# Performance work log

Hardware: AMD Instinct MI355X
Metric: run time of the kernel (lower is better)

## Reference

```python
import jax, jax.numpy as jnp
import numpy as np

B, T, N, D = 16, 48, 256, 64
K_HEADS = 8


def setup_inputs() -> dict:
    key = jax.random.key(0)
    ks = jax.random.split(key, 12)
    return {
        "query": jax.random.normal(ks[0], (B, T, N, D), jnp.float32),
        "key": jax.random.normal(ks[1], (B, T, N, D), jnp.float32),
        "value": jax.random.normal(ks[2], (B, T, N, D), jnp.float32),
        "key_w": jax.random.normal(ks[3], (B, T, D, D), jnp.float32) * 0.05,
        "key_b": jax.random.normal(ks[4], (B, T, D), jnp.float32) * 0.05,
        "value_w": jax.random.normal(ks[5], (B, T, D, D), jnp.float32) * 0.05,
        "value_b": jax.random.normal(ks[6], (B, T, D), jnp.float32) * 0.05,
        "proj1_w": jax.random.normal(ks[7], (D, D), jnp.float32) * 0.05,
        "proj1_b": jax.random.normal(ks[8], (D,), jnp.float32) * 0.05,
        "proj2_w": jax.random.normal(ks[9], (D, D), jnp.float32) * 0.05,
        "proj2_b": jax.random.normal(ks[10], (D,), jnp.float32) * 0.05,
        "rate": jnp.full((1,), 0.8, jnp.float32),
    }


def reference(query, key, value, key_w, key_b, value_w, value_b,
              proj1_w, proj1_b, proj2_w, proj2_b, rate):
    b, t, n, d = query.shape
    hs = d // K_HEADS
    # per-(batch,time) projections (LinearCustom)
    k = jnp.einsum('btnd,btde->btne', key, key_w) + key_b[:, :, None, :]
    v = jnp.einsum('btnd,btde->btne', value, value_w) + value_b[:, :, None, :]
    # split heads along channel dim (matches torch.split on dim -1)
    qh = query.reshape(b, t, n, K_HEADS, hs)
    kh = k.reshape(b, t, n, K_HEADS, hs)
    vh = v.reshape(b, t, n, K_HEADS, hs)
    # scores: [b, h, n, q, k]
    scores = jnp.einsum('bqnhd,bknhd->bhnqk', qh, kh) / jnp.sqrt(jnp.asarray(hs, query.dtype))
    # time decay: b_time_decays[..., i, j] = (T-1-i) + 1 = T - i (depends on query pos only)
    dec = (t - jnp.arange(t, dtype=scores.dtype))[:, None]  # [T, 1], broadcasts over key axis
    s = jax.nn.sigmoid(scores)
    denom = 1.0 + jax.nn.sigmoid(s * jax.nn.sigmoid(rate) * dec)
    att = jax.nn.softmax(jnp.tanh(s / denom), axis=-1)
    x = jnp.einsum('bhnqk,bknhd->bqnhd', att, vh).reshape(b, t, n, d)
    x = jnp.tanh(x @ proj1_w.T + proj1_b)
    return x @ proj2_w.T + proj2_b
```

## Files before the change

### kernel.cpp

```cpp
#include <hip/hip_runtime.h>


#define B_ 16
#define T_ 48
#define N_ 256
#define D_ 64
#define H_ 8
#define HS_ 8

__device__ __forceinline__ float rcpf(float x) { return __builtin_amdgcn_rcpf(x); }
__device__ __forceinline__ float ex2(float x) { return __builtin_amdgcn_exp2f(x); }

#define LOG2E 1.4426950408889634f

__global__ __launch_bounds__(256) void proj_kv_kernel(
    const float* __restrict__ key, const float* __restrict__ key_w, const float* __restrict__ key_b,
    const float* __restrict__ value, const float* __restrict__ value_w, const float* __restrict__ value_b,
    float* __restrict__ k_out, float* __restrict__ v_out)
{
    const int bt = blockIdx.x;
    const int which = blockIdx.y;
    const float* __restrict__ in = (which ? value : key) + (size_t)bt * N_ * D_;
    const float* __restrict__ w  = (which ? value_w : key_w) + (size_t)bt * D_ * D_;
    const float* __restrict__ bb = (which ? value_b : key_b) + (size_t)bt * D_;
    float* __restrict__ out = (which ? v_out : k_out) + (size_t)bt * N_ * D_;

    __shared__ float Wl[D_][D_];
    __shared__ float Xl[128][68];
    __shared__ float Bl[D_];

    const int tid = threadIdx.x;
    #pragma unroll
    for (int i = tid; i < D_ * D_; i += 256) Wl[i >> 6][i & 63] = w[i];
    if (tid < D_) Bl[tid] = bb[tid];

    const int cg = tid & 7;
    const int rg = tid >> 3;

    for (int n0 = 0; n0 < N_; n0 += 128) {
        __syncthreads();
        #pragma unroll
        for (int i = tid; i < 128 * D_ / 4; i += 256) {
            const int e = i * 4;
            *(float4*)&Xl[e >> 6][e & 63] = *(const float4*)&in[(size_t)n0 * D_ + e];
        }
        __syncthreads();

        float acc[4][8];
        #pragma unroll
        for (int j = 0; j < 4; ++j)
            #pragma unroll
            for (int i = 0; i < 8; ++i) acc[j][i] = Bl[cg * 8 + i];

        #pragma unroll 8
        for (int d = 0; d < D_; ++d) {
            const float4 w0 = *(const float4*)&Wl[d][cg * 8];
            const float4 w1 = *(const float4*)&Wl[d][cg * 8 + 4];
            #pragma unroll
            for (int j = 0; j < 4; ++j) {
                const float a = Xl[rg + 32 * j][d];
                acc[j][0] += a * w0.x; acc[j][1] += a * w0.y;
                acc[j][2] += a * w0.z; acc[j][3] += a * w0.w;
                acc[j][4] += a * w1.x; acc[j][5] += a * w1.y;
                acc[j][6] += a * w1.z; acc[j][7] += a * w1.w;
            }
        }

        #pragma unroll
        for (int j = 0; j < 4; ++j) {
            const size_t row = (size_t)(n0 + rg + 32 * j);
            *(float4*)&out[row * D_ + cg * 8]     = make_float4(acc[j][0], acc[j][1], acc[j][2], acc[j][3]);
            *(float4*)&out[row * D_ + cg * 8 + 4] = make_float4(acc[j][4], acc[j][5], acc[j][6], acc[j][7]);
        }
    }
}

__global__ __launch_bounds__(384) void attn_kernel(
    const float* __restrict__ query, float* __restrict__ k_xatt, const float* __restrict__ v_in,
    const float* __restrict__ rate)
{
    const int b = blockIdx.x >> 8;
    const int n = blockIdx.x & 255;

    __shared__ float Q[T_][68];
    __shared__ float K[T_][68];
    __shared__ float V[T_][68];

    const int tid = threadIdx.x;
    #pragma unroll
    for (int i = tid; i < T_ * D_ / 4; i += 384) {
        const int e = i * 4;
        const int t = e >> 6, d = e & 63;
        const size_t g = ((size_t)(b * T_ + t) * N_ + n) * D_ + d;
        *(float4*)&Q[t][d] = *(const float4*)&query[g];
        *(float4*)&K[t][d] = *(const float4*)&k_xatt[g];
        *(float4*)&V[t][d] = *(const float4*)&v_in[g];
    }
    const float rsig = rcpf(1.0f + ex2(-rate[0] * LOG2E));
    __syncthreads();

    const int q = tid % 48;
    const int h = tid / 48;

    const float C1 = 0.35355339059327373f * LOG2E;
    float4 qa = *(const float4*)&Q[q][h * 8];
    float4 qb = *(const float4*)&Q[q][h * 8 + 4];
    qa.x *= -C1; qa.y *= -C1; qa.z *= -C1; qa.w *= -C1;
    qb.x *= -C1; qb.y *= -C1; qb.z *= -C1; qb.w *= -C1;
    const float rdn = -rsig * (float)(T_ - q) * LOG2E;

    float4 acc0 = make_float4(0.f, 0.f, 0.f, 0.f);
    float4 acc1 = make_float4(0.f, 0.f, 0.f, 0.f);
    float ssum = 0.f;
    #pragma unroll 4
    for (int tk = 0; tk < T_; ++tk) {
        const float4 ka = *(const float4*)&K[tk][h * 8];
        const float4 kb = *(const float4*)&K[tk][h * 8 + 4];
        const float dn = qa.x * ka.x + qa.y * ka.y + qa.z * ka.z + qa.w * ka.w
                       + qb.x * kb.x + qb.y * kb.y + qb.z * kb.z + qb.w * kb.w;
        const float s   = rcpf(1.0f + ex2(dn));
        const float s2  = rcpf(1.0f + ex2(s * rdn));
        const float arg = s * rcpf(1.0f + s2);
        const float th  = 1.0f - 2.0f * rcpf(ex2(arg * (2.0f * LOG2E)) + 1.0f);
        const float e   = ex2(th * LOG2E);
        ssum += e;
        const float4 va = *(const float4*)&V[tk][h * 8];
        const float4 vb = *(const float4*)&V[tk][h * 8 + 4];
        acc0.x += e * va.x; acc0.y += e * va.y; acc0.z += e * va.z; acc0.w += e * va.w;
        acc1.x += e * vb.x; acc1.y += e * vb.y; acc1.z += e * vb.z; acc1.w += e * vb.w;
    }
    const float inv = rcpf(ssum);

    __syncthreads();
    acc0.x *= inv; acc0.y *= inv; acc0.z *= inv; acc0.w *= inv;
    acc1.x *= inv; acc1.y *= inv; acc1.z *= inv; acc1.w *= inv;
    *(float4*)&Q[q][h * 8]     = acc0;
    *(float4*)&Q[q][h * 8 + 4] = acc1;
    __syncthreads();

    #pragma unroll
    for (int i = tid; i < T_ * D_ / 4; i += 384) {
        const int e = i * 4;
        const int t = e >> 6, d = e & 63;
        *(float4*)&k_xatt[((size_t)(b * T_ + t) * N_ + n) * D_ + d] = *(const float4*)&Q[t][d];
    }
}

__global__ __launch_bounds__(512) void out_proj_kernel(
    const float* __restrict__ xatt,
    const float* __restrict__ p1w, const float* __restrict__ p1b,
    const float* __restrict__ p2w, const float* __restrict__ p2b,
    float* __restrict__ out)
{
    __shared__ float W1t[D_][68];
    __shared__ float W2t[D_][68];
    __shared__ float X[128][68];
    __shared__ float B1[D_], B2[D_];

    const int tid = threadIdx.x;
    const size_t m0 = (size_t)blockIdx.x * 128;

    #pragma unroll
    for (int i = tid; i < D_ * D_; i += 512) {
        const int c = i >> 6, d = i & 63;
        W1t[d][c] = p1w[i];
        W2t[d][c] = p2w[i];
    }
    #pragma unroll
    for (int i = tid; i < 128 * D_ / 4; i += 512) {
        const int e = i * 4;
        *(float4*)&X[e >> 6][e & 63] = *(const float4*)&xatt[m0 * D_ + e];
    }
    if (tid < D_) { B1[tid] = p1b[tid]; B2[tid] = p2b[tid]; }
    __syncthreads();

    const int cg = tid & 7;
    const int rp = tid >> 3;

    float x1a[8], x1b[8];
    {
        float a[8], b2r[8];
        #pragma unroll
        for (int i = 0; i < 8; ++i) { a[i] = B1[cg * 8 + i]; b2r[i] = B1[cg * 8 + i]; }
        #pragma unroll 8
        for (int d = 0; d < D_; ++d) {
            const float xv0 = X[rp][d];
            const float xv1 = X[rp + 64][d];
            const float4 w0 = *(const float4*)&W1t[d][cg * 8];
            const float4 w1 = *(const float4*)&W1t[d][cg * 8 + 4];
            a[0] += xv0 * w0.x; a[1] += xv0 * w0.y; a[2] += xv0 * w0.z; a[3] += xv0 * w0.w;
            a[4] += xv0 * w1.x; a[5] += xv0 * w1.y; a[6] += xv0 * w1.z; a[7] += xv0 * w1.w;
            b2r[0] += xv1 * w0.x; b2r[1] += xv1 * w0.y; b2r[2] += xv1 * w0.z; b2r[3] += xv1 * w0.w;
            b2r[4] += xv1 * w1.x; b2r[5] += xv1 * w1.y; b2r[6] += xv1 * w1.z; b2r[7] += xv1 * w1.w;
        }
        #pragma unroll
        for (int i = 0; i < 8; ++i) {
            x1a[i] = 1.0f - 2.0f * rcpf(ex2(a[i]   * (2.0f * LOG2E)) + 1.0f);
            x1b[i] = 1.0f - 2.0f * rcpf(ex2(b2r[i] * (2.0f * LOG2E)) + 1.0f);
        }
    }
    __syncthreads();
    #pragma unroll
    for (int i = 0; i < 8; ++i) {
        X[rp][cg * 8 + i]      = x1a[i];
        X[rp + 64][cg * 8 + i] = x1b[i];
    }
    __syncthreads();

    {
        float a[8], b2r[8];
        #pragma unroll
        for (int i = 0; i < 8; ++i) { a[i] = B2[cg * 8 + i]; b2r[i] = B2[cg * 8 + i]; }
        #pragma unroll 8
        for (int d = 0; d < D_; ++d) {
            const float xv0 = X[rp][d];
            const float xv1 = X[rp + 64][d];
            const float4 w0 = *(const float4*)&W2t[d][cg * 8];
            const float4 w1 = *(const float4*)&W2t[d][cg * 8 + 4];
            a[0] += xv0 * w0.x; a[1] += xv0 * w0.y; a[2] += xv0 * w0.z; a[3] += xv0 * w0.w;
            a[4] += xv0 * w1.x; a[5] += xv0 * w1.y; a[6] += xv0 * w1.z; a[7] += xv0 * w1.w;
            b2r[0] += xv1 * w0.x; b2r[1] += xv1 * w0.y; b2r[2] += xv1 * w0.z; b2r[3] += xv1 * w0.w;
            b2r[4] += xv1 * w1.x; b2r[5] += xv1 * w1.y; b2r[6] += xv1 * w1.z; b2r[7] += xv1 * w1.w;
        }
        const size_t og0 = (m0 + rp) * D_ + cg * 8;
        const size_t og1 = (m0 + rp + 64) * D_ + cg * 8;
        *(float4*)&out[og0]     = make_float4(a[0], a[1], a[2], a[3]);
        *(float4*)&out[og0 + 4] = make_float4(a[4], a[5], a[6], a[7]);
        *(float4*)&out[og1]     = make_float4(b2r[0], b2r[1], b2r[2], b2r[3]);
        *(float4*)&out[og1 + 4] = make_float4(b2r[4], b2r[5], b2r[6], b2r[7]);
    }
}

extern "C" void kernel_launch(void* const* d_in, const int* in_sizes, int n_in,
                              void* d_out, int out_size, void* d_ws, size_t ws_size,
                              hipStream_t stream) {
    const float* query   = (const float*)d_in[0];
    const float* key     = (const float*)d_in[1];
    const float* value   = (const float*)d_in[2];
    const float* key_w   = (const float*)d_in[3];
    const float* key_b   = (const float*)d_in[4];
    const float* value_w = (const float*)d_in[5];
    const float* value_b = (const float*)d_in[6];
    const float* p1w     = (const float*)d_in[7];
    const float* p1b     = (const float*)d_in[8];
    const float* p2w     = (const float*)d_in[9];
    const float* p2b     = (const float*)d_in[10];
    const float* rate    = (const float*)d_in[11];
    float* out = (float*)d_out;

    float* kws = (float*)d_ws;
    float* vws = kws + (size_t)B_ * T_ * N_ * D_;

    dim3 gridA(B_ * T_, 2);
    proj_kv_kernel<<<gridA, 256, 0, stream>>>(key, key_w, key_b, value, value_w, value_b, kws, vws);
    attn_kernel<<<B_ * N_, 384, 0, stream>>>(query, kws, vws, rate);
    out_proj_kernel<<<(B_ * T_ * N_) / 128, 512, 0, stream>>>(kws, p1w, p1b, p2w, p2b, out);
}
```

Measured before the change: 222.8 us.

## Register-tile attention over four queries per thread and enlarge out-proj tiles

The attention kernel now gives each block two nodes and each thread four queries of one head. Each K/V row read from shared memory is reused across four query computations, queries are read straight from global memory, and outputs are written directly. The output projection kernel drops to 128 threads, each computing an 8x8 register tile with float4 X loads, which raises reuse of each shared-memory read. The cost is higher register pressure and fewer threads per block, which may reduce occupancy and latency hiding, especially with the exp-heavy attention loop.

```diff
diff --git a/kernel.cpp b/kernel.cpp
--- a/kernel.cpp
+++ b/kernel.cpp
@@ -75,159 +75,197 @@
     }
 }
 
-__global__ __launch_bounds__(384) void attn_kernel(
+__global__ __launch_bounds__(192) void attn_kernel(
     const float* __restrict__ query, float* __restrict__ k_xatt, const float* __restrict__ v_in,
     const float* __restrict__ rate)
 {
-    const int b = blockIdx.x >> 8;
-    const int n = blockIdx.x & 255;
-
-    __shared__ float Q[T_][68];
-    __shared__ float K[T_][68];
-    __shared__ float V[T_][68];
+    const int b  = blockIdx.x >> 7;
+    const int n0 = (blockIdx.x & 127) * 2;
+
+    __shared__ float K[2][T_][D_];
+    __shared__ float V[2][T_][D_];
 
     const int tid = threadIdx.x;
     #pragma unroll
-    for (int i = tid; i < T_ * D_ / 4; i += 384) {
-        const int e = i * 4;
-        const int t = e >> 6, d = e & 63;
-        const size_t g = ((size_t)(b * T_ + t) * N_ + n) * D_ + d;
-        *(float4*)&Q[t][d] = *(const float4*)&query[g];
-        *(float4*)&K[t][d] = *(const float4*)&k_xatt[g];
-        *(float4*)&V[t][d] = *(const float4*)&v_in[g];
+    for (int i = tid; i < T_ * 16; i += 192) {
+        const int t = i >> 4, d4 = (i & 15) * 4;
+        const size_t g0 = ((size_t)(b * T_ + t) * N_ + n0) * D_ + d4;
+        *(float4*)&K[0][t][d4] = *(const float4*)&k_xatt[g0];
+        *(float4*)&V[0][t][d4] = *(const float4*)&v_in[g0];
+        *(float4*)&K[1][t][d4] = *(const float4*)&k_xatt[g0 + D_];
+        *(float4*)&V[1][t][d4] = *(const float4*)&v_in[g0 + D_];
     }
     const float rsig = rcpf(1.0f + ex2(-rate[0] * LOG2E));
-    __syncthreads();
-
-    const int q = tid % 48;
-    const int h = tid / 48;
+
+    const int nl  = tid / 96;
+    const int r96 = tid % 96;
+    const int qg  = r96 >> 3;
+    const int h   = r96 & 7;
+    const int n   = n0 + nl;
 
     const float C1 = 0.35355339059327373f * LOG2E;
-    float4 qa = *(const float4*)&Q[q][h * 8];
-    float4 qb = *(const float4*)&Q[q][h * 8 + 4];
-    qa.x *= -C1; qa.y *= -C1; qa.z *= -C1; qa.w *= -C1;
-    qb.x *= -C1; qb.y *= -C1; qb.z *= -C1; qb.w *= -C1;
-    const float rdn = -rsig * (float)(T_ - q) * LOG2E;
-
-    float4 acc0 = make_float4(0.f, 0.f, 0.f, 0.f);
-    float4 acc1 = make_float4(0.f, 0.f, 0.f, 0.f);
-    float ssum = 0.f;
-    #pragma unroll 4
+    float4 qa[4], qb[4];
+    float rdn[4];
+    #pragma unroll
+    for (int j = 0; j < 4; ++j) {
+        const int q = qg + 12 * j;
+        const size_t g = ((size_t)(b * T_ + q) * N_ + n) * D_ + h * 8;
+        const float4 a = *(const float4*)&query[g];
+        const float4 c = *(const float4*)&query[g + 4];
+        qa[j] = make_float4(-C1 * a.x, -C1 * a.y, -C1 * a.z, -C1 * a.w);
+        qb[j] = make_float4(-C1 * c.x, -C1 * c.y, -C1 * c.z, -C1 * c.w);
+        rdn[j] = -rsig * (float)(T_ - q) * LOG2E;
+    }
+    __syncthreads();
+
+    float4 acc0[4], acc1[4];
+    float ssum[4];
+    #pragma unroll
+    for (int j = 0; j < 4; ++j) {
+        acc0[j] = make_float4(0.f, 0.f, 0.f, 0.f);
+        acc1[j] = make_float4(0.f, 0.f, 0.f, 0.f);
+        ssum[j] = 0.f;
+    }
+
+    #pragma unroll 2
     for (int tk = 0; tk < T_; ++tk) {
-        const float4 ka = *(const float4*)&K[tk][h * 8];
-        const float4 kb = *(const float4*)&K[tk][h * 8 + 4];
-        const float dn = qa.x * ka.x + qa.y * ka.y + qa.z * ka.z + qa.w * ka.w
-                       + qb.x * kb.x + qb.y * kb.y + qb.z * kb.z + qb.w * kb.w;
-        const float s   = rcpf(1.0f + ex2(dn));
-        const float s2  = rcpf(1.0f + ex2(s * rdn));
-        const float arg = s * rcpf(1.0f + s2);
-        const float th  = 1.0f - 2.0f * rcpf(ex2(arg * (2.0f * LOG2E)) + 1.0f);
-        const float e   = ex2(th * LOG2E);
-        ssum += e;
-        const float4 va = *(const float4*)&V[tk][h * 8];
-        const float4 vb = *(const float4*)&V[tk][h * 8 + 4];
-        acc0.x += e * va.x; acc0.y += e * va.y; acc0.z += e * va.z; acc0.w += e * va.w;
-        acc1.x += e * vb.x; acc1.y += e * vb.y; acc1.z += e * vb.z; acc1.w += e * vb.w;
-    }
-    const float inv = rcpf(ssum);
-
-    __syncthreads();
-    acc0.x *= inv; acc0.y *= inv; acc0.z *= inv; acc0.w *= inv;
-    acc1.x *= inv; acc1.y *= inv; acc1.z *= inv; acc1.w *= inv;
-    *(float4*)&Q[q][h * 8]     = acc0;
-    *(float4*)&Q[q][h * 8 + 4] = acc1;
-    __syncthreads();
-
-    #pragma unroll
-    for (int i = tid; i < T_ * D_ / 4; i += 384) {
-        const int e = i * 4;
-        const int t = e >> 6, d = e & 63;
-        *(float4*)&k_xatt[((size_t)(b * T_ + t) * N_ + n) * D_ + d] = *(const float4*)&Q[t][d];
-    }
-}
-
-__global__ __launch_bounds__(512) void out_proj_kernel(
+        const float4 ka = *(const float4*)&K[nl][tk][h * 8];
+        const float4 kb = *(const float4*)&K[nl][tk][h * 8 + 4];
+        const float4 va = *(const float4*)&V[nl][tk][h * 8];
+        const float4 vb = *(const float4*)&V[nl][tk][h * 8 + 4];
+        #pragma unroll
+        for (int j = 0; j < 4; ++j) {
+            const float dn = qa[j].x * ka.x + qa[j].y * ka.y + qa[j].z * ka.z + qa[j].w * ka.w
+                           + qb[j].x * kb.x + qb[j].y * kb.y + qb[j].z * kb.z + qb[j].w * kb.w;
+            const float s   = rcpf(1.0f + ex2(dn));
+            const float s2  = rcpf(1.0f + ex2(s * rdn[j]));
+            const float arg = s * rcpf(1.0f + s2);
+            const float th  = 1.0f - 2.0f * rcpf(ex2(arg * (2.0f * LOG2E)) + 1.0f);
+            const float e   = ex2(th * LOG2E);
+            ssum[j] += e;
+            acc0[j].x += e * va.x; acc0[j].y += e * va.y; acc0[j].z += e * va.z; acc0[j].w += e * va.w;
+            acc1[j].x += e * vb.x; acc1[j].y += e * vb.y; acc1[j].z += e * vb.z; acc1[j].w += e * vb.w;
+        }
+    }
+
+    #pragma unroll
+    for (int j = 0; j < 4; ++j) {
+        const float inv = rcpf(ssum[j]);
+        const int q = qg + 12 * j;
+        const size_t g = ((size_t)(b * T_ + q) * N_ + n) * D_ + h * 8;
+        *(float4*)&k_xatt[g]     = make_float4(acc0[j].x * inv, acc0[j].y * inv, acc0[j].z * inv, acc0[j].w * inv);
+        *(float4*)&k_xatt[g + 4] = make_float4(acc1[j].x * inv, acc1[j].y * inv, acc1[j].z * inv, acc1[j].w * inv);
+    }
+}
+
+__global__ __launch_bounds__(128) void out_proj_kernel(
     const float* __restrict__ xatt,
     const float* __restrict__ p1w, const float* __restrict__ p1b,
     const float* __restrict__ p2w, const float* __restrict__ p2b,
     float* __restrict__ out)
 {
+    __shared__ float X[128][68];
     __shared__ float W1t[D_][68];
     __shared__ float W2t[D_][68];
-    __shared__ float X[128][68];
     __shared__ float B1[D_], B2[D_];
 
     const int tid = threadIdx.x;
     const size_t m0 = (size_t)blockIdx.x * 128;
 
     #pragma unroll
-    for (int i = tid; i < D_ * D_; i += 512) {
+    for (int i = tid; i < D_ * D_; i += 128) {
         const int c = i >> 6, d = i & 63;
         W1t[d][c] = p1w[i];
         W2t[d][c] = p2w[i];
     }
     #pragma unroll
-    for (int i = tid; i < 128 * D_ / 4; i += 512) {
-        const int e = i * 4;
-        *(float4*)&X[e >> 6][e & 63] = *(const float4*)&xatt[m0 * D_ + e];
+    for (int i = tid; i < 128 * 16; i += 128) {
+        const int row = i >> 4, d4 = (i & 15) * 4;
+        *(float4*)&X[row][d4] = *(const float4*)&xatt[(m0 + row) * D_ + d4];
     }
     if (tid < D_) { B1[tid] = p1b[tid]; B2[tid] = p2b[tid]; }
     __syncthreads();
 
     const int cg = tid & 7;
-    const int rp = tid >> 3;
-
-    float x1a[8], x1b[8];
+    const int rg = tid >> 3;
+
+    float x1[8][8];
     {
-        float a[8], b2r[8];
-        #pragma unroll
-        for (int i = 0; i < 8; ++i) { a[i] = B1[cg * 8 + i]; b2r[i] = B1[cg * 8 + i]; }
-        #pragma unroll 8
-        for (int d = 0; d < D_; ++d) {
-            const float xv0 = X[rp][d];
-            const float xv1 = X[rp + 64][d];
-            const float4 w0 = *(const float4*)&W1t[d][cg * 8];
-            const float4 w1 = *(const float4*)&W1t[d][cg * 8 + 4];
-            a[0] += xv0 * w0.x; a[1] += xv0 * w0.y; a[2] += xv0 * w0.z; a[3] += xv0 * w0.w;
-            a[4] += xv0 * w1.x; a[5] += xv0 * w1.y; a[6] += xv0 * w1.z; a[7] += xv0 * w1.w;
-            b2r[0] += xv1 * w0.x; b2r[1] += xv1 * w0.y; b2r[2] += xv1 * w0.z; b2r[3] += xv1 * w0.w;
-            b2r[4] += xv1 * w1.x; b2r[5] += xv1 * w1.y; b2r[6] += xv1 * w1.z; b2r[7] += xv1 * w1.w;
-        }
-        #pragma unroll
-        for (int i = 0; i < 8; ++i) {
-            x1a[i] = 1.0f - 2.0f * rcpf(ex2(a[i]   * (2.0f * LOG2E)) + 1.0f);
-            x1b[i] = 1.0f - 2.0f * rcpf(ex2(b2r[i] * (2.0f * LOG2E)) + 1.0f);
-        }
-    }
-    __syncthreads();
-    #pragma unroll
-    for (int i = 0; i < 8; ++i) {
-        X[rp][cg * 8 + i]      = x1a[i];
-        X[rp + 64][cg * 8 + i] = x1b[i];
+        float acc[8][8];
+        #pragma unroll
+        for (int j = 0; j < 8; ++j)
+            #pragma unroll
+            for (int i = 0; i < 8; ++i) acc[j][i] = B1[cg * 8 + i];
+
+        #pragma unroll 4
+        for (int d0 = 0; d0 < D_; d0 += 4) {
+            float4 w0[4], w1[4];
+            #pragma unroll
+            for (int dd = 0; dd < 4; ++dd) {
+                w0[dd] = *(const float4*)&W1t[d0 + dd][cg * 8];
+                w1[dd] = *(const float4*)&W1t[d0 + dd][cg * 8 + 4];
+            }
+            #pragma unroll
+            for (int j = 0; j < 8; ++j) {
+                const float4 xv = *(const float4*)&X[rg + 16 * j][d0];
+                acc[j][0] += xv.x * w0[0].x + xv.y * w0[1].x + xv.z * w0[2].x + xv.w * w0[3].x;
+                acc[j][1] += xv.x * w0[0].y + xv.y * w0[1].y + xv.z * w0[2].y + xv.w * w0[3].y;
+                acc[j][2] += xv.x * w0[0].z + xv.y * w0[1].z + xv.z * w0[2].z + xv.w * w0[3].z;
+                acc[j][3] += xv.x * w0[0].w + xv.y * w0[1].w + xv.z * w0[2].w + xv.w * w0[3].w;
+                acc[j][4] += xv.x * w1[0].x + xv.y * w1[1].x + xv.z * w1[2].x + xv.w * w1[3].x;
+                acc[j][5] += xv.x * w1[0].y + xv.y * w1[1].y + xv.z * w1[2].y + xv.w * w1[3].y;
+                acc[j][6] += xv.x * w1[0].z + xv.y * w1[1].z + xv.z * w1[2].z + xv.w * w1[3].z;
+                acc[j][7] += xv.x * w1[0].w + xv.y * w1[1].w + xv.z * w1[2].w + xv.w * w1[3].w;
+            }
+        }
+        #pragma unroll
+        for (int j = 0; j < 8; ++j)
+            #pragma unroll
+            for (int i = 0; i < 8; ++i)
+                x1[j][i] = 1.0f - 2.0f * rcpf(ex2(acc[j][i] * (2.0f * LOG2E)) + 1.0f);
+    }
+    __syncthreads();
+    #pragma unroll
+    for (int j = 0; j < 8; ++j) {
+        *(float4*)&X[rg + 16 * j][cg * 8]     = make_float4(x1[j][0], x1[j][1], x1[j][2], x1[j][3]);
+        *(float4*)&X[rg + 16 * j][cg * 8 + 4] = make_float4(x1[j][4], x1[j][5], x1[j][6], x1[j][7]);
     }
     __syncthreads();
 
     {
-        float a[8], b2r[8];
-        #pragma unroll
-        for (int i = 0; i < 8; ++i) { a[i] = B2[cg * 8 + i]; b2r[i] = B2[cg * 8 + i]; }
-        #pragma unroll 8
-        for (int d = 0; d < D_; ++d) {
-            const float xv0 = X[rp][d];
-            const float xv1 = X[rp + 64][d];
-            const float4 w0 = *(const float4*)&W2t[d][cg * 8];
-            const float4 w1 = *(const float4*)&W2t[d][cg * 8 + 4];
-            a[0] += xv0 * w0.x; a[1] += xv0 * w0.y; a[2] += xv0 * w0.z; a[3] += xv0 * w0.w;
-            a[4] += xv0 * w1.x; a[5] += xv0 * w1.y; a[6] += xv0 * w1.z; a[7] += xv0 * w1.w;
-            b2r[0] += xv1 * w0.x; b2r[1] += xv1 * w0.y; b2r[2] += xv1 * w0.z; b2r[3] += xv1 * w0.w;
-            b2r[4] += xv1 * w1.x; b2r[5] += xv1 * w1.y; b2r[6] += xv1 * w1.z; b2r[7] += xv1 * w1.w;
-        }
-        const size_t og0 = (m0 + rp) * D_ + cg * 8;
-        const size_t og1 = (m0 + rp + 64) * D_ + cg * 8;
-        *(float4*)&out[og0]     = make_float4(a[0], a[1], a[2], a[3]);
-        *(float4*)&out[og0 + 4] = make_float4(a[4], a[5], a[6], a[7]);
-        *(float4*)&out[og1]     = make_float4(b2r[0], b2r[1], b2r[2], b2r[3]);
-        *(float4*)&out[og1 + 4] = make_float4(b2r[4], b2r[5], b2r[6], b2r[7]);
+        float acc[8][8];
+        #pragma unroll
+        for (int j = 0; j < 8; ++j)
+            #pragma unroll
+            for (int i = 0; i < 8; ++i) acc[j][i] = B2[cg * 8 + i];
+
+        #pragma unroll 4
+        for (int d0 = 0; d0 < D_; d0 += 4) {
+            float4 w0[4], w1[4];
+            #pragma unroll
+            for (int dd = 0; dd < 4; ++dd) {
+                w0[dd] = *(const float4*)&W2t[d0 + dd][cg * 8];
+                w1[dd] = *(const float4*)&W2t[d0 + dd][cg * 8 + 4];
+            }
+            #pragma unroll
+            for (int j = 0; j < 8; ++j) {
+                const float4 xv = *(const float4*)&X[rg + 16 * j][d0];
+                acc[j][0] += xv.x * w0[0].x + xv.y * w0[1].x + xv.z * w0[2].x + xv.w * w0[3].x;
+                acc[j][1] += xv.x * w0[0].y + xv.y * w0[1].y + xv.z * w0[2].y + xv.w * w0[3].y;
+                acc[j][2] += xv.x * w0[0].z + xv.y * w0[1].z + xv.z * w0[2].z + xv.w * w0[3].z;
+                acc[j][3] += xv.x * w0[0].w + xv.y * w0[1].w + xv.z * w0[2].w + xv.w * w0[3].w;
+                acc[j][4] += xv.x * w1[0].x + xv.y * w1[1].x + xv.z * w1[2].x + xv.w * w1[3].x;
+                acc[j][5] += xv.x * w1[0].y + xv.y * w1[1].y + xv.z * w1[2].y + xv.w * w1[3].y;
+                acc[j][6] += xv.x * w1[0].z + xv.y * w1[1].z + xv.z * w1[2].z + xv.w * w1[3].z;
+                acc[j][7] += xv.x * w1[0].w + xv.y * w1[1].w + xv.z * w1[2].w + xv.w * w1[3].w;
+            }
+        }
+        #pragma unroll
+        for (int j = 0; j < 8; ++j) {
+            const size_t og = (m0 + rg + 16 * j) * D_ + cg * 8;
+            *(float4*)&out[og]     = make_float4(acc[j][0], acc[j][1], acc[j][2], acc[j][3]);
+            *(float4*)&out[og + 4] = make_float4(acc[j][4], acc[j][5], acc[j][6], acc[j][7]);
+        }
     }
 }
 
@@ -253,6 +291,6 @@
 
     dim3 gridA(B_ * T_, 2);
     proj_kv_kernel<<<gridA, 256, 0, stream>>>(key, key_w, key_b, value, value_w, value_b, kws, vws);
-    attn_kernel<<<B_ * N_, 384, 0, stream>>>(query, kws, vws, rate);
-    out_proj_kernel<<<(B_ * T_ * N_) / 128, 512, 0, stream>>>(kws, p1w, p1b, p2w, p2b, out);
-}
+    attn_kernel<<<B_ * (N_ / 2), 192, 0, stream>>>(query, kws, vws, rate);
+    out_proj_kernel<<<(B_ * T_ * N_) / 128, 128, 0, stream>>>(kws, p1w, p1b, p2w, p2b, out);
+}
```

Result: slower. 276.2 us (+24.0%).
